# Optimization experiments

Hardware: AMD Instinct MI355X
Metric: run time of the kernel (lower is better)

Reference implementation:

```python
import jax, jax.numpy as jnp
import numpy as np

EPSILON = 1e-8
PSD_EPS = 1e-5


def _mask_norm(mask):
    # torch.norm(mask, inf, dim=1, keepdim=True): max |.| over F axis
    max_abs = jnp.max(jnp.abs(mask), axis=1, keepdims=True)
    return mask / (max_abs + EPSILON)


def _estimate_psd(mask, cm):
    # mask: [B,F,T] real; cm: [B,C,F,T] complex -> psd [B,F,C,C]
    x = jnp.transpose(cm, (0, 2, 1, 3))            # [B,F,C,T]
    m = mask[:, :, None, :]                        # [B,F,1,T]
    nom = jnp.einsum('bfct,bfdt->bfcd', x * m, jnp.conj(x))
    den = jnp.clip(jnp.sum(m, axis=-1, keepdims=True), PSD_EPS, None)
    psd = nom / den
    return psd + 1j * jnp.asarray(PSD_EPS, psd.real.dtype)


def setup_inputs() -> dict:
    key = jax.random.key(0)
    k1, k2, k3, k4 = jax.random.split(key, 4)
    B, C, F, T = 8, 8, 257, 1500
    return {
        'speech_mask': jax.random.uniform(k1, (B, F, T), dtype=jnp.float32),
        'noise_mask': jax.random.uniform(k2, (B, F, T), dtype=jnp.float32),
        'cm_real': jax.random.normal(k3, (B, C, F, T), dtype=jnp.float32),
        'cm_imag': jax.random.normal(k4, (B, C, F, T), dtype=jnp.float32),
    }


def reference(speech_mask, noise_mask, cm_real, cm_imag):
    eps = EPSILON
    cm = cm_real + 1j * cm_imag                    # [B,C,F,T] complex64
    B, C, F, T = cm.shape

    sm = _mask_norm(speech_mask)
    nm = _mask_norm(noise_mask)

    speech_psd = _estimate_psd(sm, cm) + 1j * jnp.float32(eps)   # [B,F,C,C]
    noise_psd = _estimate_psd(nm, cm) + 1j * jnp.float32(eps)

    # diagonal loading + inverse, stabilized
    eye = jnp.eye(C, dtype=noise_psd.dtype)
    noise_psd_inv = jnp.linalg.inv(noise_psd + eye * eps)
    noise_psd_inv = noise_psd_inv + 1j * jnp.float32(eps)

    A = noise_psd_inv @ speech_psd                 # [B,F,C,C]
    tr = jnp.einsum('bfcc->bf', A) + eps           # trace [B,F]

    ref_vec = jnp.zeros((B, C), dtype=A.dtype).at[:, 0].set(1.0)
    u = jnp.einsum('bfcd,bd->bfc', A, ref_vec)     # [B,F,C]
    weight = u / tr[..., None]                     # [B,F,C]
    w = jnp.transpose(weight, (0, 2, 1))           # [B,C,F]

    # apply beamformer: sum_c conj(w) * cm -> [B,F,T]
    out = jnp.einsum('bcf,bcft->bft', jnp.conj(w), cm)
    return jnp.stack([out.real, out.imag])         # [2,B,F,T] float32
```

## Files before the change

kernel.cpp:

```cpp
#include <hip/hip_runtime.h>

#define Bb 8
#define Cc 8
#define Ff 257
#define Tt 1500
#define P2 750
#define BF (Bb*Ff)

__device__ __forceinline__ constexpr int utIdx(int c, int d) { return c*(17-c)/2 + (d-c); }
__device__ __forceinline__ constexpr int odIdx(int c, int d) { return 7*c - c*(c-1)/2 + (d-c-1); }

constexpr float EPSv   = 1e-8f;
constexpr float PSDEPS = 1e-5f;
constexpr float IMADD  = 1e-5f + 1e-8f;

__global__ void mask_pmax(const float* __restrict__ sm, const float* __restrict__ nm,
                          float* __restrict__ pmax_s, float* __restrict__ pmax_n) {
    int t  = blockIdx.x * 256 + threadIdx.x;
    int ch = blockIdx.y;
    int b  = blockIdx.z;
    if (t >= Tt) return;
    int f0 = ch * 33, f1 = min(Ff, f0 + 33);
    float ms = 0.f, mn = 0.f;
    for (int f = f0; f < f1; ++f) {
        ms = fmaxf(ms, fabsf(sm[(b*Ff + f)*Tt + t]));
        mn = fmaxf(mn, fabsf(nm[(b*Ff + f)*Tt + t]));
    }
    pmax_s[(b*8 + ch)*Tt + t] = ms;
    pmax_n[(b*8 + ch)*Tt + t] = mn;
}

__global__ void mask_inv(const float* __restrict__ pmax_s, const float* __restrict__ pmax_n,
                         float* __restrict__ inv_s, float* __restrict__ inv_n) {
    int t = blockIdx.x * 256 + threadIdx.x;
    int b = blockIdx.y;
    if (t >= Tt) return;
    float ms = 0.f, mn = 0.f;
    #pragma unroll
    for (int ch = 0; ch < 8; ++ch) {
        ms = fmaxf(ms, pmax_s[(b*8 + ch)*Tt + t]);
        mn = fmaxf(mn, pmax_n[(b*8 + ch)*Tt + t]);
    }
    inv_s[b*Tt + t] = 1.0f / (ms + EPSv);
    inv_n[b*Tt + t] = 1.0f / (mn + EPSv);
}

__global__ __launch_bounds__(256, 3) void mvdr_main(
    const float* __restrict__ smask, const float* __restrict__ nmask,
    const float* __restrict__ cmr,   const float* __restrict__ cmi,
    const float* __restrict__ inv_s, const float* __restrict__ inv_n,
    float* __restrict__ out)
{
    const int blk = blockIdx.x;
    const int b = blk / Ff, f = blk % Ff;
    const int tid  = threadIdx.x;
    const int par  = tid & 1;
    const int pair = tid >> 1;
    const int wid  = tid >> 6;
    const int lane = tid & 63;

    const float2* sm2 = (const float2*)smask + (b*Ff + f)*P2;
    const float2* nm2 = (const float2*)nmask + (b*Ff + f)*P2;
    const float2* is2 = (const float2*)inv_s + b*P2;
    const float2* in2 = (const float2*)inv_n + b*P2;
    const float2* m2  = par ? nm2 : sm2;
    const float2* iv2 = par ? in2 : is2;
    const int cstride = Ff * P2;
    const float2* xr2 = (const float2*)cmr + (b*Cc)*cstride + f*P2;
    const float2* xi2 = (const float2*)cmi + (b*Cc)*cstride + f*P2;

    float acc[64];
    #pragma unroll
    for (int v = 0; v < 64; ++v) acc[v] = 0.f;
    float summ = 0.f;

    int p = pair;
    #pragma unroll 1
    for (int it = 0; it < 6; ++it, p += 128) {
        if (p < P2) {
            float2 mk = m2[p], iv = iv2[p];
            float2 xr[8], xi[8];
            #pragma unroll
            for (int c = 0; c < 8; ++c) { xr[c] = xr2[p + c*cstride]; xi[c] = xi2[p + c*cstride]; }
            float mx = mk.x * iv.x, my = mk.y * iv.y;
            summ += mx + my;
            #pragma unroll
            for (int c = 0; c < 8; ++c) {
                float ax = mx*xr[c].x, ay = my*xr[c].y, bx = mx*xi[c].x, by = my*xi[c].y;
                {
                    const int k = utIdx(c, c);
                    float t0 = acc[k];
                    t0 = fmaf(ax, xr[c].x, t0); t0 = fmaf(bx, xi[c].x, t0);
                    t0 = fmaf(ay, xr[c].y, t0); t0 = fmaf(by, xi[c].y, t0);
                    acc[k] = t0;
                }
                #pragma unroll
                for (int d = c + 1; d < 8; ++d) {
                    const int k = utIdx(c, d);
                    const int j = 36 + odIdx(c, d);
                    float t0 = acc[k], t1 = acc[j];
                    t0 = fmaf(ax, xr[d].x, t0); t0 = fmaf(bx, xi[d].x, t0);
                    t0 = fmaf(ay, xr[d].y, t0); t0 = fmaf(by, xi[d].y, t0);
                    t1 = fmaf(bx, xr[d].x, t1); t1 = fmaf(-ax, xi[d].x, t1);
                    t1 = fmaf(by, xr[d].y, t1); t1 = fmaf(-ay, xi[d].y, t1);
                    acc[k] = t0; acc[j] = t1;
                }
            }
        }
    }

    #pragma unroll
    for (int o = 2; o <= 32; o <<= 1) summ += __shfl_xor(summ, o, 64);
    __shared__ float msum[4], nsum[4];
    if (lane == 0) msum[wid] = summ;
    if (lane == 1) nsum[wid] = summ;

    #pragma unroll
    for (int v = 0; v < 64; ++v) {
        acc[v] += __shfl_xor(acc[v], 2, 64);
        acc[v] += __shfl_xor(acc[v], 4, 64);
    }
    __shared__ float red[64*36];
    const int col = wid*8 + (lane >> 3);
    if (par == 0 && (lane & 7) == 0) {
        #pragma unroll
        for (int v = 0; v < 64; ++v) red[v*36 + col] = acc[v];
    }
    __syncthreads();
    float Sval = 0.f;
    if (tid < 64) {
        const float4* row = (const float4*)(red + tid*36);
        #pragma unroll
        for (int k = 0; k < 8; ++k) { float4 r4 = row[k]; Sval += r4.x + r4.y + r4.z + r4.w; }
    }
    __syncthreads();
    if (par == 1 && (lane & 7) == 1) {
        #pragma unroll
        for (int v = 0; v < 64; ++v) red[v*36 + col] = acc[v];
    }
    __syncthreads();
    float Nval = 0.f;
    if (tid < 64) {
        const float4* row = (const float4*)(red + tid*36);
        #pragma unroll
        for (int k = 0; k < 8; ++k) { float4 r4 = row[k]; Nval += r4.x + r4.y + r4.z + r4.w; }
    }

    __shared__ float SreM[64], SimM[64];
    __shared__ float Are[128], Aim[128];
    __shared__ float dre[8], dim_[8], wre[8], wim[8];

    if (tid < 64) {
        const float den_s = fmaxf(msum[0]+msum[1]+msum[2]+msum[3], PSDEPS);
        const float den_n = fmaxf(nsum[0]+nsum[1]+nsum[2]+nsum[3], PSDEPS);
        int cc_, dd_;
        if (tid < 36) { int k = tid, c = 0; while (k >= 8 - c) { k -= 8 - c; ++c; } cc_ = c; dd_ = c + k; }
        else          { int k = tid - 36, c = 0; while (k >= 7 - c) { k -= 7 - c; ++c; } cc_ = c; dd_ = c + k + 1; }
        float sv = Sval / den_s, nv = Nval / den_n;
        if (tid < 36) {
            SreM[cc_*8 + dd_] = sv; SreM[dd_*8 + cc_] = sv;
            float nvd = nv + (cc_ == dd_ ? EPSv : 0.f);
            Are[cc_*16 + dd_] = nvd; Are[dd_*16 + cc_] = nvd;
            if (cc_ == dd_) { SimM[cc_*8 + cc_] = IMADD; Aim[cc_*16 + cc_] = IMADD; }
        } else {
            SimM[cc_*8 + dd_] = IMADD + sv; SimM[dd_*8 + cc_] = IMADD - sv;
            Aim[cc_*16 + dd_] = IMADD + nv; Aim[dd_*16 + cc_] = IMADD - nv;
        }
        int r = tid >> 3, j = tid & 7;
        Are[r*16 + 8 + j] = (r == j) ? 1.f : 0.f;
        Aim[r*16 + 8 + j] = 0.f;
    }
    __syncthreads();

    {
        const bool act = tid < 64;
        const int r = (tid >> 3) & 7, cA = tid & 7;
        for (int k = 0; k < 8; ++k) {
            float pr = Are[k*16 + k], pi = Aim[k*16 + k];
            float idn = 1.0f / (pr*pr + pi*pi);
            float ipr = pr*idn, ipi = -pi*idn;
            if (act && r == k) {
                float ar0 = Are[k*16 + cA],     ai0 = Aim[k*16 + cA];
                Are[k*16 + cA]     = ar0*ipr - ai0*ipi; Aim[k*16 + cA]     = ar0*ipi + ai0*ipr;
                float ar1 = Are[k*16 + cA + 8], ai1 = Aim[k*16 + cA + 8];
                Are[k*16 + cA + 8] = ar1*ipr - ai1*ipi; Aim[k*16 + cA + 8] = ar1*ipi + ai1*ipr;
            }
            __syncthreads();
            float fr = Are[r*16 + k], fi = Aim[r*16 + k];
            float p0r = Are[k*16 + cA],     p0i = Aim[k*16 + cA];
            float p1r = Are[k*16 + cA + 8], p1i = Aim[k*16 + cA + 8];
            float o0r = 0.f, o0i = 0.f, o1r = 0.f, o1i = 0.f;
            if (r != k) {
                o0r = Are[r*16 + cA]     - (fr*p0r - fi*p0i);
                o0i = Aim[r*16 + cA]     - (fr*p0i + fi*p0r);
                o1r = Are[r*16 + cA + 8] - (fr*p1r - fi*p1i);
                o1i = Aim[r*16 + cA + 8] - (fr*p1i + fi*p1r);
            }
            __syncthreads();
            if (act && r != k) {
                Are[r*16 + cA]     = o0r; Aim[r*16 + cA]     = o0i;
                Are[r*16 + cA + 8] = o1r; Aim[r*16 + cA + 8] = o1i;
            }
            __syncthreads();
        }
    }

    if (tid < 8) {
        int c = tid;
        float ur = 0.f, ui = 0.f, tr_r = 0.f, tr_i = 0.f;
        #pragma unroll
        for (int j = 0; j < 8; ++j) {
            float vr = Are[c*16 + 8 + j], vi = Aim[c*16 + 8 + j] + EPSv;
            float s0r = SreM[j*8 + 0], s0i = SimM[j*8 + 0];
            ur += vr*s0r - vi*s0i; ui += vr*s0i + vi*s0r;
            float scr = SreM[j*8 + c], sci = SimM[j*8 + c];
            tr_r += vr*scr - vi*sci; tr_i += vr*sci + vi*scr;
        }
        dre[c] = tr_r; dim_[c] = tr_i;
        wre[c] = ur;   wim[c]  = ui;
    }
    __syncthreads();
    if (tid < 8) {
        float tr_r = EPSv, tr_i = 0.f;
        #pragma unroll
        for (int j = 0; j < 8; ++j) { tr_r += dre[j]; tr_i += dim_[j]; }
        float idn = 1.0f / (tr_r*tr_r + tr_i*tr_i);
        float ur = wre[tid], ui = wim[tid];
        wre[tid] = (ur*tr_r + ui*tr_i) * idn;
        wim[tid] = (ui*tr_r - ur*tr_i) * idn;
    }
    __syncthreads();

    float wr[8], wi[8];
    #pragma unroll
    for (int c = 0; c < 8; ++c) { wr[c] = wre[c]; wi[c] = wim[c]; }

    float2* outr = (float2*)out + (b*Ff + f)*P2;
    float2* outi = (float2*)out + (Bb*Ff)*P2 + (b*Ff + f)*P2;
    for (int pp = tid; pp < P2; pp += 256) {
        float rx = 0.f, ry = 0.f, ix = 0.f, iy = 0.f;
        #pragma unroll
        for (int c = 0; c < 8; ++c) {
            float2 a  = xr2[pp + c*cstride];
            float2 bb = xi2[pp + c*cstride];
            rx += wr[c]*a.x + wi[c]*bb.x;
            ry += wr[c]*a.y + wi[c]*bb.y;
            ix += wr[c]*bb.x - wi[c]*a.x;
            iy += wr[c]*bb.y - wi[c]*a.y;
        }
        outr[pp] = make_float2(rx, ry);
        outi[pp] = make_float2(ix, iy);
    }
}

extern "C" void kernel_launch(void* const* d_in, const int* in_sizes, int n_in,
                              void* d_out, int out_size, void* d_ws, size_t ws_size,
                              hipStream_t stream) {
    const float* smask = (const float*)d_in[0];
    const float* nmask = (const float*)d_in[1];
    const float* cmr   = (const float*)d_in[2];
    const float* cmi   = (const float*)d_in[3];
    float* ws = (float*)d_ws;
    float* pmax_s = ws;
    float* pmax_n = ws + 96000;
    float* inv_s  = ws + 192000;
    float* inv_n  = ws + 204000;

    mask_pmax<<<dim3(6, 8, 8), 256, 0, stream>>>(smask, nmask, pmax_s, pmax_n);
    mask_inv <<<dim3(6, 8),    256, 0, stream>>>(pmax_s, pmax_n, inv_s, inv_n);
    mvdr_main<<<BF, 256, 0, stream>>>(smask, nmask, cmr, cmi, inv_s, inv_n, (float*)d_out);
}
```

Measured before the change: 301.4 us.

## Split PSD accumulation into real/imag roles to cut registers and reduction cost

Each thread now handles one of four roles (speech or noise mask, real or imaginary part) over 36 upper-triangular accumulators instead of 64. This halves register pressure so occupancy can rise from 3 to 4 waves per SIMD, and replaces the two-pass shared-memory reduction with wave shuffles plus one small shared buffer. The trade-off is that each thread reloads the same channel data for its role, doubling the number of time-pair iterations per thread, and the diagonal imaginary entries are computed redundantly.

After: 329.3 us. 1.09x slower.

```diff
diff --git a/kernel.cpp b/kernel.cpp
--- a/kernel.cpp
+++ b/kernel.cpp
@@ -8,7 +8,6 @@
 #define BF (Bb*Ff)
 
 __device__ __forceinline__ constexpr int utIdx(int c, int d) { return c*(17-c)/2 + (d-c); }
-__device__ __forceinline__ constexpr int odIdx(int c, int d) { return 7*c - c*(c-1)/2 + (d-c-1); }
 
 constexpr float EPSv   = 1e-8f;
 constexpr float PSDEPS = 1e-5f;
@@ -45,7 +44,7 @@
     inv_n[b*Tt + t] = 1.0f / (mn + EPSv);
 }
 
-__global__ __launch_bounds__(256, 3) void mvdr_main(
+__global__ __launch_bounds__(256, 4) void mvdr_main(
     const float* __restrict__ smask, const float* __restrict__ nmask,
     const float* __restrict__ cmr,   const float* __restrict__ cmi,
     const float* __restrict__ inv_s, const float* __restrict__ inv_n,
@@ -54,8 +53,9 @@
     const int blk = blockIdx.x;
     const int b = blk / Ff, f = blk % Ff;
     const int tid  = threadIdx.x;
-    const int par  = tid & 1;
-    const int pair = tid >> 1;
+    const int role = tid & 3;
+    const int part = role & 1;
+    const int quad = tid >> 2;
     const int wid  = tid >> 6;
     const int lane = tid & 63;
 
@@ -63,20 +63,20 @@
     const float2* nm2 = (const float2*)nmask + (b*Ff + f)*P2;
     const float2* is2 = (const float2*)inv_s + b*P2;
     const float2* in2 = (const float2*)inv_n + b*P2;
-    const float2* m2  = par ? nm2 : sm2;
-    const float2* iv2 = par ? in2 : is2;
+    const float2* m2  = (role & 2) ? nm2 : sm2;
+    const float2* iv2 = (role & 2) ? in2 : is2;
     const int cstride = Ff * P2;
     const float2* xr2 = (const float2*)cmr + (b*Cc)*cstride + f*P2;
     const float2* xi2 = (const float2*)cmi + (b*Cc)*cstride + f*P2;
 
-    float acc[64];
-    #pragma unroll
-    for (int v = 0; v < 64; ++v) acc[v] = 0.f;
+    float acc[36];
+    #pragma unroll
+    for (int v = 0; v < 36; ++v) acc[v] = 0.f;
     float summ = 0.f;
 
-    int p = pair;
+    int p = quad;
     #pragma unroll 1
-    for (int it = 0; it < 6; ++it, p += 128) {
+    for (int it = 0; it < 12; ++it, p += 64) {
         if (p < P2) {
             float2 mk = m2[p], iv = iv2[p];
             float2 xr[8], xi[8];
@@ -84,67 +84,49 @@
             for (int c = 0; c < 8; ++c) { xr[c] = xr2[p + c*cstride]; xi[c] = xi2[p + c*cstride]; }
             float mx = mk.x * iv.x, my = mk.y * iv.y;
             summ += mx + my;
+            float mxn = part ? -mx : mx;
+            float myn = part ? -my : my;
             #pragma unroll
             for (int c = 0; c < 8; ++c) {
-                float ax = mx*xr[c].x, ay = my*xr[c].y, bx = mx*xi[c].x, by = my*xi[c].y;
-                {
-                    const int k = utIdx(c, c);
+                float u1 = part ? xi[c].x : xr[c].x;
+                float u2 = part ? xi[c].y : xr[c].y;
+                float v1 = part ? xr[c].x : xi[c].x;
+                float v2 = part ? xr[c].y : xi[c].y;
+                float A1 = mx*u1, A2 = my*u2, C1 = mxn*v1, C2 = myn*v2;
+                #pragma unroll
+                for (int d = c; d < 8; ++d) {
+                    const int k = utIdx(c, d);
                     float t0 = acc[k];
-                    t0 = fmaf(ax, xr[c].x, t0); t0 = fmaf(bx, xi[c].x, t0);
-                    t0 = fmaf(ay, xr[c].y, t0); t0 = fmaf(by, xi[c].y, t0);
+                    t0 = fmaf(A1, xr[d].x, t0);
+                    t0 = fmaf(C1, xi[d].x, t0);
+                    t0 = fmaf(A2, xr[d].y, t0);
+                    t0 = fmaf(C2, xi[d].y, t0);
                     acc[k] = t0;
                 }
-                #pragma unroll
-                for (int d = c + 1; d < 8; ++d) {
-                    const int k = utIdx(c, d);
-                    const int j = 36 + odIdx(c, d);
-                    float t0 = acc[k], t1 = acc[j];
-                    t0 = fmaf(ax, xr[d].x, t0); t0 = fmaf(bx, xi[d].x, t0);
-                    t0 = fmaf(ay, xr[d].y, t0); t0 = fmaf(by, xi[d].y, t0);
-                    t1 = fmaf(bx, xr[d].x, t1); t1 = fmaf(-ax, xi[d].x, t1);
-                    t1 = fmaf(by, xr[d].y, t1); t1 = fmaf(-ay, xi[d].y, t1);
-                    acc[k] = t0; acc[j] = t1;
-                }
-            }
-        }
-    }
-
-    #pragma unroll
-    for (int o = 2; o <= 32; o <<= 1) summ += __shfl_xor(summ, o, 64);
+            }
+        }
+    }
+
+    #pragma unroll
+    for (int o = 4; o <= 32; o <<= 1) summ += __shfl_xor(summ, o, 64);
+    #pragma unroll
+    for (int v = 0; v < 36; ++v) {
+        acc[v] += __shfl_xor(acc[v], 4, 64);
+        acc[v] += __shfl_xor(acc[v], 8, 64);
+        acc[v] += __shfl_xor(acc[v], 16, 64);
+        acc[v] += __shfl_xor(acc[v], 32, 64);
+    }
+
     __shared__ float msum[4], nsum[4];
+    __shared__ float red[16*36];
     if (lane == 0) msum[wid] = summ;
-    if (lane == 1) nsum[wid] = summ;
-
-    #pragma unroll
-    for (int v = 0; v < 64; ++v) {
-        acc[v] += __shfl_xor(acc[v], 2, 64);
-        acc[v] += __shfl_xor(acc[v], 4, 64);
-    }
-    __shared__ float red[64*36];
-    const int col = wid*8 + (lane >> 3);
-    if (par == 0 && (lane & 7) == 0) {
-        #pragma unroll
-        for (int v = 0; v < 64; ++v) red[v*36 + col] = acc[v];
-    }
-    __syncthreads();
-    float Sval = 0.f;
-    if (tid < 64) {
-        const float4* row = (const float4*)(red + tid*36);
-        #pragma unroll
-        for (int k = 0; k < 8; ++k) { float4 r4 = row[k]; Sval += r4.x + r4.y + r4.z + r4.w; }
-    }
-    __syncthreads();
-    if (par == 1 && (lane & 7) == 1) {
-        #pragma unroll
-        for (int v = 0; v < 64; ++v) red[v*36 + col] = acc[v];
-    }
-    __syncthreads();
-    float Nval = 0.f;
-    if (tid < 64) {
-        const float4* row = (const float4*)(red + tid*36);
-        #pragma unroll
-        for (int k = 0; k < 8; ++k) { float4 r4 = row[k]; Nval += r4.x + r4.y + r4.z + r4.w; }
-    }
+    if (lane == 2) nsum[wid] = summ;
+    if (lane < 4) {
+        const int row = wid*4 + lane;
+        #pragma unroll
+        for (int v = 0; v < 36; ++v) red[row*36 + v] = acc[v];
+    }
+    __syncthreads();
 
     __shared__ float SreM[64], SimM[64];
     __shared__ float Are[128], Aim[128];
@@ -153,16 +135,24 @@
     if (tid < 64) {
         const float den_s = fmaxf(msum[0]+msum[1]+msum[2]+msum[3], PSDEPS);
         const float den_n = fmaxf(nsum[0]+nsum[1]+nsum[2]+nsum[3], PSDEPS);
-        int cc_, dd_;
-        if (tid < 36) { int k = tid, c = 0; while (k >= 8 - c) { k -= 8 - c; ++c; } cc_ = c; dd_ = c + k; }
-        else          { int k = tid - 36, c = 0; while (k >= 7 - c) { k -= 7 - c; ++c; } cc_ = c; dd_ = c + k + 1; }
-        float sv = Sval / den_s, nv = Nval / den_n;
         if (tid < 36) {
+            int k = tid, c = 0; while (k >= 8 - c) { k -= 8 - c; ++c; }
+            const int cc_ = c, dd_ = c + k;
+            const int ki = tid;
+            float Sval = red[0*36+ki] + red[4*36+ki] + red[8*36+ki] + red[12*36+ki];
+            float Nval = red[2*36+ki] + red[6*36+ki] + red[10*36+ki] + red[14*36+ki];
+            float sv = Sval / den_s, nv = Nval / den_n;
             SreM[cc_*8 + dd_] = sv; SreM[dd_*8 + cc_] = sv;
             float nvd = nv + (cc_ == dd_ ? EPSv : 0.f);
             Are[cc_*16 + dd_] = nvd; Are[dd_*16 + cc_] = nvd;
             if (cc_ == dd_) { SimM[cc_*8 + cc_] = IMADD; Aim[cc_*16 + cc_] = IMADD; }
         } else {
+            int k = tid - 36, c = 0; while (k >= 7 - c) { k -= 7 - c; ++c; }
+            const int cc_ = c, dd_ = c + k + 1;
+            const int ki = utIdx(cc_, dd_);
+            float Sval = red[1*36+ki] + red[5*36+ki] + red[9*36+ki] + red[13*36+ki];
+            float Nval = red[3*36+ki] + red[7*36+ki] + red[11*36+ki] + red[15*36+ki];
+            float sv = Sval / den_s, nv = Nval / den_n;
             SimM[cc_*8 + dd_] = IMADD + sv; SimM[dd_*8 + cc_] = IMADD - sv;
             Aim[cc_*16 + dd_] = IMADD + nv; Aim[dd_*16 + cc_] = IMADD - nv;
         }
```
